# Kernel tuning notes

Hardware: AMD Instinct MI355X
Metric: run time of the kernel (lower is better)

## Reference

```python
import jax, jax.numpy as jnp
import numpy as np
from jax.scipy.linalg import solve_triangular

B, L, HID, NH = 2, 1024, 1024, 4
DK = DV = 256
CONV_K, CHUNK, FIR_S_K, FIR_L_K = 4, 32, 3, 31
GATE_IN = HID + 3 * DV * 4 + DV * 4  # 5120
GATE_H = 2 * DV  # 512


def _l2norm(x):
    return x * jax.lax.rsqrt(jnp.sum(x * x, -1, keepdims=True) + 1e-6)


def _short_conv(x, w):
    # causal depthwise conv1d + silu. x: [b,l,c], w: [c,k]
    c, k = w.shape
    y = jax.lax.conv_general_dilated(x.transpose(0, 2, 1), w[:, None, :], (1,),
                                     [(k - 1, 0)], feature_group_count=c)
    return jax.nn.silu(y.transpose(0, 2, 1))


def _fir(x, f):
    # per-head depthwise causal FIR. x: [b,l,h,d], f: [h,d,k]
    b, l, h, d = x.shape
    k = f.shape[-1]
    xf = x.transpose(0, 2, 3, 1).reshape(b, h * d, l)
    y = jax.lax.conv_general_dilated(xf, f.reshape(h * d, 1, k), (1,),
                                     [(k - 1, 0)], feature_group_count=h * d)
    return y.reshape(b, h, d, l).transpose(0, 3, 1, 2)


def _delta_rule(q, k, v, beta, chunk=CHUNK):
    # q,k: [b,h,L,dk], v: [b,h,L,dv], beta: [b,h,L]; L % chunk == 0
    b, h, l, dk = q.shape
    dv = v.shape[-1]
    n = l // chunk
    q = _l2norm(q)
    k = _l2norm(k)
    v = v * beta[..., None]
    kb = k * beta[..., None]
    rs = lambda t: t.reshape(b, h, n, chunk, -1)
    q, k, v, kb = map(rs, (q, k, v, kb))
    # UT transform: serial forward substitution == unit-lower triangular solve
    A = -jnp.tril(jnp.einsum('bhncd,bhned->bhnce', kb, k), -1)  # strictly lower
    eye = jnp.eye(chunk, dtype=q.dtype)
    T = solve_triangular(eye - A, jnp.broadcast_to(eye, A.shape), lower=True)
    u = T @ v   # [b,h,n,c,dv]
    w = T @ kb  # [b,h,n,c,dk]
    mov = lambda t: jnp.moveaxis(t, 2, 0)

    def step(S, inp):
        qi, ki, ui, wi = inp  # [b,h,c,d]
        attn = jnp.tril(qi @ ki.transpose(0, 1, 3, 2))  # causal incl. diag
        u_i = ui - wi @ S
        o_i = qi @ S + attn @ u_i
        return S + ki.transpose(0, 1, 3, 2) @ u_i, o_i

    S0 = jnp.zeros((b, h, dk, dv), dtype=q.dtype)
    S, o = jax.lax.scan(step, S0, (mov(q), mov(k), mov(u), mov(w)))
    o = jnp.moveaxis(o, 0, 2).reshape(b, h, l, dv)
    return o, S


def _gate(hidden, branches, W1, b1, W2, b2, temp, eps_floor):
    def stats(p):
        m = p.mean(-1, keepdims=True)
        r = jnp.sqrt(jnp.clip((p * p).mean(-1, keepdims=True), 1e-8))
        mx = p.max(-1, keepdims=True)
        return jnp.concatenate([jnp.broadcast_to(m, p.shape),
                                jnp.broadcast_to(r, p.shape),
                                jnp.broadcast_to(mx, p.shape)], -1)

    b, l, h, d = branches[0].shape
    hb = jnp.broadcast_to(hidden[:, :, None, :], (b, l, h, hidden.shape[-1]))
    head_in = jnp.concatenate([hb] + [stats(p) for p in branches] + list(branches), -1)
    hmid = jax.nn.gelu(head_in @ W1 + b1, approximate=False)
    logits = hmid @ W2 + b2  # [b,l,h,4]
    t = jnp.clip(temp, 0.2, 10.0)[None, None, :, None]
    w = jax.nn.softmax(logits / t, -1)
    floor = jnp.clip(eps_floor, 1e-7, 0.1)[None, None]
    w = jnp.maximum(w, floor)
    return w / w.sum(-1, keepdims=True)


def setup_inputs() -> dict:
    key = jax.random.key(0)
    ks = jax.random.split(key, 16)
    s = 0.02
    inp = {
        'x': jax.random.normal(ks[0], (B, L, HID), jnp.float32),
        'Wq': jax.random.normal(ks[1], (HID, NH * DK), jnp.float32) * s,
        'Wk': jax.random.normal(ks[2], (HID, NH * DK), jnp.float32) * s,
        'Wv': jax.random.normal(ks[3], (HID, NH * DV), jnp.float32) * s,
        'Wb': jax.random.normal(ks[4], (HID, NH), jnp.float32) * s,
        'qc_w': jax.random.normal(ks[5], (NH * DK, CONV_K), jnp.float32) * 0.5,
        'kc_w': jax.random.normal(ks[6], (NH * DK, CONV_K), jnp.float32) * 0.5,
        'vc_w': jax.random.normal(ks[7], (NH * DV, CONV_K), jnp.float32) * 0.5,
        'gW1': jax.random.normal(ks[10], (GATE_IN, GATE_H), jnp.float32) * s,
        'gb1': jnp.zeros((GATE_H,), jnp.float32),
        'gW2': jax.random.normal(ks[11], (GATE_H, 4), jnp.float32) * s,
        'gb2': jnp.zeros((4,), jnp.float32),
        'temp': jnp.ones((NH,), jnp.float32),
        'eps_floor': jnp.full((NH, 4), 0.01, jnp.float32),
        'onorm_w': jnp.ones((DV,), jnp.float32),
        'Wo': jax.random.normal(ks[12], (NH * DV, HID), jnp.float32) * s,
    }
    # FIR filters: identity tap at last position + small noise (matches init intent)
    fs = jnp.zeros((NH, DV, FIR_S_K)).at[..., -1].set(1.0)
    fl = jnp.zeros((NH, DV, FIR_L_K)).at[..., -1].set(1.0)
    inp['fir_s'] = fs + s * jax.random.normal(ks[8], fs.shape, jnp.float32)
    inp['fir_l'] = fl + s * jax.random.normal(ks[9], fl.shape, jnp.float32)
    return inp


def reference(x, Wq, Wk, Wv, Wb, qc_w, kc_w, vc_w, fir_s, fir_l,
              gW1, gb1, gW2, gb2, temp, eps_floor, onorm_w, Wo):
    b, l, _ = x.shape
    q = _short_conv(x @ Wq, qc_w).reshape(b, l, NH, DK)
    k = _short_conv(x @ Wk, kc_w).reshape(b, l, NH, DK)
    v = _short_conv(x @ Wv, vc_w).reshape(b, l, NH, DV)
    beta = jax.nn.sigmoid(x @ Wb)  # [b,l,h]
    tr = lambda t: t.transpose(0, 2, 1, 3)
    delta_o, _ = _delta_rule(tr(q), tr(k), tr(v), beta.transpose(0, 2, 1))
    delta_o = tr(delta_o)  # [b,l,h,dv]
    branches = [_fir(v, fir_s), _fir(v, fir_l), delta_o, v]
    w = _gate(x, branches, gW1, gb1, gW2, gb2, temp, eps_floor)
    o = sum(w[..., i:i + 1] * branches[i] for i in range(4))
    o = o * jax.lax.rsqrt((o * o).mean(-1, keepdims=True) + 1e-5) * onorm_w
    return o.reshape(b, l, NH * DV) @ Wo
```

## Files before the change

kernel.cpp:

```cpp
#include <hip/hip_runtime.h>
#include <math.h>

#define BB 2
#define LL 1024
#define HIDD 1024
#define NH 4
#define DD 256
#define NCH 32
#define ROWS 2048
#define HROWS 8192

typedef long long i64;
typedef unsigned short u16t;
typedef unsigned int u32t;
typedef __attribute__((ext_vector_type(8))) short short8;
typedef __attribute__((ext_vector_type(4))) float f32x4;
#define MFMA_BF16(a, b, c) __builtin_amdgcn_mfma_f32_16x16x32_bf16(a, b, c, 0, 0, 0)

__device__ __forceinline__ float sigmoidf_(float x) { return 1.0f / (1.0f + expf(-x)); }

__device__ __forceinline__ u16t f2bf(float f) {
  u32t u = __float_as_uint(f);
  u = u + 0x7FFFu + ((u >> 16) & 1u);
  return (u16t)(u >> 16);
}
__device__ __forceinline__ u32t pk2(u16t a, u16t b) { return (u32t)a | ((u32t)b << 16); }

__device__ __forceinline__ void barrier_lds_only() {
  asm volatile("s_waitcnt lgkmcnt(0)" ::: "memory");
  __builtin_amdgcn_s_barrier();
  asm volatile("" ::: "memory");
}

template<int N>
__device__ __forceinline__ void block_reduce_sum(float* v, float* scratch) {
  int lane = threadIdx.x & 63, wid = threadIdx.x >> 6;
#pragma unroll
  for (int i = 0; i < N; i++) {
    float x = v[i];
#pragma unroll
    for (int off = 1; off < 64; off <<= 1) x += __shfl_xor(x, off);
    if (lane == 0) scratch[wid * N + i] = x;
  }
  __syncthreads();
#pragma unroll
  for (int i = 0; i < N; i++)
    v[i] = scratch[i] + scratch[N + i] + scratch[2 * N + i] + scratch[3 * N + i];
  __syncthreads();
}

template<int N>
__device__ __forceinline__ void block_reduce_max(float* v, float* scratch) {
  int lane = threadIdx.x & 63, wid = threadIdx.x >> 6;
#pragma unroll
  for (int i = 0; i < N; i++) {
    float x = v[i];
#pragma unroll
    for (int off = 1; off < 64; off <<= 1) x = fmaxf(x, __shfl_xor(x, off));
    if (lane == 0) scratch[wid * N + i] = x;
  }
  __syncthreads();
#pragma unroll
  for (int i = 0; i < N; i++)
    v[i] = fmaxf(fmaxf(scratch[i], scratch[N + i]),
                 fmaxf(scratch[2 * N + i], scratch[3 * N + i]));
  __syncthreads();
}

__device__ __forceinline__ void transcast_body(
    const float* __restrict__ in, int ldin, u16t* __restrict__ out, int ldout,
    int nbi, int kbi, float (*tile)[33]) {
  int tx = threadIdx.x & 31, ty = threadIdx.x >> 5;
  int nb = nbi * 32, kb = kbi * 32;
#pragma unroll
  for (int r = 0; r < 4; r++)
    tile[ty + r * 8][tx] = in[(i64)(kb + ty + r * 8) * ldin + nb + tx];
  __syncthreads();
#pragma unroll
  for (int r = 0; r < 4; r++)
    out[(i64)(nb + ty + r * 8) * ldout + kb + tx] = f2bf(tile[tx][ty + r * 8]);
}

__global__ __launch_bounds__(256) void prep_kernel(
    const float* __restrict__ Wq, const float* __restrict__ Wk, const float* __restrict__ Wv,
    const float* __restrict__ x,
    u16t* __restrict__ WqkvT, u16t* __restrict__ xbf) {
  __shared__ float tile[32][33];
  int blk = blockIdx.x, t = threadIdx.x;
  if (blk < 3072) {
    int m = blk >> 10, bi = blk & 1023;
    const float* in = m == 0 ? Wq : m == 1 ? Wk : Wv;
    transcast_body(in, 1024, WqkvT + (i64)m * 1024 * 1024, 1024, bi & 31, bi >> 5, tile);
  } else {
    i64 e = ((i64)(blk - 3072) * 256 + t) * 4;
    float4 v = *(const float4*)(x + e);
    uint2 o;
    o.x = pk2(f2bf(v.x), f2bf(v.y));
    o.y = pk2(f2bf(v.z), f2bf(v.w));
    *(uint2*)(xbf + e) = o;
  }
}

__global__ __launch_bounds__(256) void prep2_kernel(
    const float* __restrict__ gW1, const float* __restrict__ Wo,
    u16t* __restrict__ W1hT, u16t* __restrict__ W1bT, u16t* __restrict__ WoT) {
  __shared__ float tile[32][33];
  int blk = blockIdx.x;
  if (blk < 1024) {
    int which = blk >> 9, bi = blk & 511;
    const float* in = gW1 + (which ? (i64)4096 * 512 : 0);
    transcast_body(in, 512, which ? W1bT : W1hT, 1024, bi & 15, bi >> 4, tile);
  } else {
    int bi = blk - 1024;
    transcast_body(Wo, 1024, WoT, 1024, bi & 31, bi >> 5, tile);
  }
}

__device__ __forceinline__ void gemm_bt_body(
    const u16t* __restrict__ A, const u16t* __restrict__ B,
    float* __restrict__ C, int K, int ldc, int n0, int m0,
    u16t* As, u16t* Bs) {
  int t = threadIdx.x;
  int w = t >> 6, lane = t & 63;
  int l15 = lane & 15, quad = lane >> 4;
  int wm = (w & 1) * 64, wn = (w >> 1) * 64;
  f32x4 acc[4][4] = {};
  int srow = t >> 1, shalf = (t & 1) * 16;
  const u16t* Ag = A + (i64)(m0 + srow) * K + shalf;
  const u16t* Bg = B + (i64)(n0 + srow) * K + shalf;
  for (int k0 = 0; k0 < K; k0 += 32) {
    *(uint4*)&As[srow * 40 + shalf] = *(const uint4*)(Ag + k0);
    *(uint4*)&As[srow * 40 + shalf + 8] = *(const uint4*)(Ag + k0 + 8);
    *(uint4*)&Bs[srow * 40 + shalf] = *(const uint4*)(Bg + k0);
    *(uint4*)&Bs[srow * 40 + shalf + 8] = *(const uint4*)(Bg + k0 + 8);
    __syncthreads();
    short8 a[4], b[4];
#pragma unroll
    for (int mt = 0; mt < 4; mt++)
      a[mt] = *(const short8*)&As[(wm + mt * 16 + l15) * 40 + quad * 8];
#pragma unroll
    for (int nt = 0; nt < 4; nt++)
      b[nt] = *(const short8*)&Bs[(wn + nt * 16 + l15) * 40 + quad * 8];
#pragma unroll
    for (int mt = 0; mt < 4; mt++)
#pragma unroll
      for (int nt = 0; nt < 4; nt++)
        acc[mt][nt] = MFMA_BF16(a[mt], b[nt], acc[mt][nt]);
    __syncthreads();
  }
#pragma unroll
  for (int mt = 0; mt < 4; mt++) {
    int r0 = m0 + wm + mt * 16 + quad * 4;
#pragma unroll
    for (int nt = 0; nt < 4; nt++) {
      int cc = n0 + wn + nt * 16 + l15;
#pragma unroll
      for (int rg = 0; rg < 4; rg++)
        C[(i64)(r0 + rg) * ldc + cc] = acc[mt][nt][rg];
    }
  }
}

__global__ __launch_bounds__(256) void gemm_bt_kernel(
    const u16t* __restrict__ A, const u16t* __restrict__ B,
    float* __restrict__ C, int K, int ldc) {
  __shared__ u16t As[128 * 40];
  __shared__ u16t Bs[128 * 40];
  gemm_bt_body(A, B, C, K, ldc, blockIdx.x * 128, blockIdx.y * 128, As, Bs);
}

__global__ __launch_bounds__(256) void conv_silu3_kernel(
    const float* __restrict__ pre, const float* __restrict__ qw,
    const float* __restrict__ kw, const float* __restrict__ vw,
    float* __restrict__ qo, float* __restrict__ ko, float* __restrict__ vo,
    u16t* __restrict__ brcat) {
  int seg = blockIdx.x >> 13;
  int idx = (blockIdx.x & 8191) * 256 + threadIdx.x;
  int c = idx & 1023, row = idx >> 10, l = row & 1023;
  const float* w = seg == 0 ? qw : seg == 1 ? kw : vw;
  float* out = seg == 0 ? qo : seg == 1 ? ko : vo;
  float4 wv = *(const float4*)(w + c * 4);
  const float* base = pre + (i64)row * 3072 + (seg << 10) + c;
  float acc = wv.w * base[0];
  if (l >= 1) acc += wv.z * base[-3072];
  if (l >= 2) acc += wv.y * base[-2 * 3072];
  if (l >= 3) acc += wv.x * base[-3 * 3072];
  float r = acc * sigmoidf_(acc);
  out[(i64)row * 1024 + c] = r;
  if (seg == 2)
    brcat[((i64)row * 4 + (c >> 8)) * 1024 + 768 + (c & 255)] = f2bf(r);
}

__global__ __launch_bounds__(256) void beta_kernel(
    const float* __restrict__ x, const float* __restrict__ Wb, float* __restrict__ beta) {
  int row = blockIdx.x, t = threadIdx.x;
  __shared__ float sc[16];
  float a[4] = {0, 0, 0, 0};
  for (int c = t; c < 1024; c += 256) {
    float xv = x[(i64)row * 1024 + c];
    float4 wv = *(const float4*)(Wb + c * 4);
    a[0] += xv * wv.x; a[1] += xv * wv.y; a[2] += xv * wv.z; a[3] += xv * wv.w;
  }
  block_reduce_sum<4>(a, sc);
  if (t == 0) {
#pragma unroll
    for (int g = 0; g < 4; g++) beta[row * 4 + g] = sigmoidf_(a[g]);
  }
}

__global__ __launch_bounds__(256) void preprocess_kernel(
    const float* __restrict__ q, const float* __restrict__ k, const float* __restrict__ v,
    const float* __restrict__ beta, float* __restrict__ qn, float* __restrict__ kn,
    float* __restrict__ vb, float* __restrict__ kb, u16t* __restrict__ qnbf) {
  int row = blockIdx.x, t = threadIdx.x;
  __shared__ float sc[8];
  i64 base = (i64)row * 256 + t;
  float qv = q[base], kv = k[base], vv = v[base];
  float vals[2] = {qv * qv, kv * kv};
  block_reduce_sum<2>(vals, sc);
  float qi = rsqrtf(vals[0] + 1e-6f), ki = rsqrtf(vals[1] + 1e-6f);
  float bet = beta[row];
  float qnv = qv * qi, knv = kv * ki;
  qn[base] = qnv;
  kn[base] = knv;
  vb[base] = vv * bet;
  kb[base] = knv * bet;
  int b = row >> 12, l = (row >> 2) & 1023, h = row & 3;
  qnbf[((i64)(b * 4 + h) * 1024 + l) * 256 + t] = f2bf(qnv);
}

__global__ __launch_bounds__(256) void phaseA_kernel(
    const float* __restrict__ qn, const float* __restrict__ kn,
    const float* __restrict__ vb, const float* __restrict__ kb,
    float* __restrict__ u_g, u16t* __restrict__ w_bf, u16t* __restrict__ attn_bf,
    u16t* __restrict__ knT) {
  __shared__ float KN[32][260];
  __shared__ float Ms[32][32];
  int blk = blockIdx.x, t = threadIdx.x;
  int i = blk & 31, bh = blk >> 5;
  int rbase = ((bh >> 2) * LL + i * 32) * NH + (bh & 3);
  i64 bhn = blk;
#pragma unroll
  for (int ii = 0; ii < 8; ii++) {
    int fid = t + ii * 256;
    int c = fid >> 6, dq = (fid & 63) << 2;
    *(float4*)&KN[c][dq] = *(const float4*)(kn + (i64)(rbase + c * NH) * 256 + dq);
  }
  __syncthreads();
  int c = t >> 3, e0 = (t & 7) * 4;
  const float* kbp = kb + (i64)(rbase + c * NH) * 256;
  const float* qp = qn + (i64)(rbase + c * NH) * 256;
  float am[4] = {0, 0, 0, 0}, aa[4] = {0, 0, 0, 0};
  for (int d = 0; d < 256; d += 4) {
    float4 kv = *(const float4*)(kbp + d);
    float4 qv = *(const float4*)(qp + d);
#pragma unroll
    for (int z = 0; z < 4; z++) {
      float4 nv = *(const float4*)&KN[e0 + z][d];
      am[z] += kv.x * nv.x + kv.y * nv.y + kv.z * nv.z + kv.w * nv.w;
      aa[z] += qv.x * nv.x + qv.y * nv.y + qv.z * nv.z + qv.w * nv.w;
    }
  }
  {
    uint2 o;
    u16t a0 = (e0 + 0 <= c) ? f2bf(aa[0]) : 0;
    u16t a1 = (e0 + 1 <= c) ? f2bf(aa[1]) : 0;
    u16t a2 = (e0 + 2 <= c) ? f2bf(aa[2]) : 0;
    u16t a3 = (e0 + 3 <= c) ? f2bf(aa[3]) : 0;
    o.x = pk2(a0, a1); o.y = pk2(a2, a3);
    *(uint2*)(attn_bf + bhn * 1024 + c * 32 + e0) = o;
  }
#pragma unroll
  for (int z = 0; z < 4; z++) {
    int e = e0 + z;
    Ms[c][e] = (e < c) ? am[z] : 0.0f;
  }
  __syncthreads();
  float uc[32], wc[32];
#pragma unroll
  for (int cc = 0; cc < 32; cc++) {
    float uval = vb[(i64)(rbase + cc * NH) * 256 + t];
    float wval = kb[(i64)(rbase + cc * NH) * 256 + t];
#pragma unroll
    for (int c2 = 0; c2 < cc; c2++) {
      float m = Ms[cc][c2];
      uval -= m * uc[c2];
      wval -= m * wc[c2];
    }
    uc[cc] = uval; wc[cc] = wval;
    u_g[(bhn * 32 + cc) * 256 + t] = uval;
    w_bf[(bhn * 32 + cc) * 256 + t] = f2bf(-wval);
  }
  int d = t;
  u16t o[32];
#pragma unroll
  for (int cc = 0; cc < 32; cc++) o[cc] = f2bf(KN[cc][d]);
#pragma unroll
  for (int z = 0; z < 4; z++) {
    uint4 vv;
    vv.x = pk2(o[z * 8 + 0], o[z * 8 + 1]);
    vv.y = pk2(o[z * 8 + 2], o[z * 8 + 3]);
    vv.z = pk2(o[z * 8 + 4], o[z * 8 + 5]);
    vv.w = pk2(o[z * 8 + 6], o[z * 8 + 7]);
    *(uint4*)(knT + (bhn * 256 + d) * 32 + z * 8) = vv;
  }
}

#define SROW 264
struct ScanBuf {
  short8 m8[8];
  f32x4 uc4;
  short8 af;
  short8 kf[4];
};

__device__ void delta_scan_body(
    int blk,
    const u16t* __restrict__ wbf, const u16t* __restrict__ knT,
    const float* __restrict__ u_g, const u16t* __restrict__ qnbf,
    const u16t* __restrict__ attnbf,
    float* __restrict__ dlt, u16t* __restrict__ brcat,
    u16t* Sbf, u16t* Ubf) {
  int t = threadIdx.x, w = t >> 6, lane = t & 63;
  int l15 = lane & 15, quad = lane >> 4;
  int bh = blk & 7, jb = blk >> 3, j0 = jb * 16;
  int b_ = bh >> 2, h_ = bh & 3;
  bool isU = (w < 2);
  int wc = isU ? w : (w - 2);
  for (int idx = t; idx < 16 * SROW; idx += 256) Sbf[idx] = 0;
  f32x4 accS[4] = {};
  __syncthreads();
  __builtin_amdgcn_s_setprio(1);

  auto load_chunk = [&](int i, ScanBuf& B) {
    i64 bhn = (i64)bh * 32 + i;
    const u16t* mbase = isU
        ? wbf + (bhn * 32 + wc * 16 + l15) * 256 + quad * 8
        : qnbf + ((i64)bh * 1024 + i * 32 + wc * 16 + l15) * 256 + quad * 8;
#pragma unroll
    for (int kd = 0; kd < 8; kd++) B.m8[kd] = *(const short8*)(mbase + kd * 32);
    if (isU) {
      int cm = wc * 16 + quad * 4;
#pragma unroll
      for (int r = 0; r < 4; r++)
        B.uc4[r] = u_g[(bhn * 32 + cm + r) * 256 + j0 + l15];
    } else {
      B.af = *(const short8*)(attnbf + bhn * 1024 + (wc * 16 + l15) * 32 + quad * 8);
    }
#pragma unroll
    for (int dt = 0; dt < 4; dt++)
      B.kf[dt] = *(const short8*)(knT + (bhn * 256 + w * 64 + dt * 16 + l15) * 32 + quad * 8);
  };

  auto process = [&](int i, ScanBuf& B) {
    f32x4 zero = {};
    f32x4 ca = isU ? B.uc4 : zero;
    f32x4 cb = zero;
#pragma unroll
    for (int kd = 0; kd < 4; kd++) {
      short8 sfa = *(const short8*)&Sbf[l15 * SROW + kd * 32 + quad * 8];
      short8 sfb = *(const short8*)&Sbf[l15 * SROW + (kd + 4) * 32 + quad * 8];
      ca = MFMA_BF16(B.m8[kd], sfa, ca);
      cb = MFMA_BF16(B.m8[kd + 4], sfb, cb);
    }
    f32x4 cacc;
#pragma unroll
    for (int r = 0; r < 4; r++) cacc[r] = ca[r] + cb[r];
    if (isU) {
      int cm = wc * 16 + quad * 4;
      uint2 o;
      o.x = pk2(f2bf(cacc[0]), f2bf(cacc[1]));
      o.y = pk2(f2bf(cacc[2]), f2bf(cacc[3]));
      *(uint2*)&Ubf[l15 * 40 + cm] = o;
    }
    barrier_lds_only();
    short8 bu = *(const short8*)&Ubf[l15 * 40 + quad * 8];
    if (!isU) {
      cacc = MFMA_BF16(B.af, bu, cacc);
#pragma unroll
      for (int rg = 0; rg < 4; rg++) {
        int l = i * 32 + wc * 16 + quad * 4 + rg;
        i64 row = ((i64)b_ * 1024 + l) * 4 + h_;
        dlt[row * 256 + j0 + l15] = cacc[rg];
        brcat[row * 1024 + 512 + j0 + l15] = f2bf(cacc[rg]);
      }
    }
#pragma unroll
    for (int dt = 0; dt < 4; dt++) accS[dt] = MFMA_BF16(B.kf[dt], bu, accS[dt]);
#pragma unroll
    for (int dt = 0; dt < 4; dt++) {
      uint2 o;
      o.x = pk2(f2bf(accS[dt][0]), f2bf(accS[dt][1]));
      o.y = pk2(f2bf(accS[dt][2]), f2bf(accS[dt][3]));
      *(uint2*)&Sbf[l15 * SROW + w * 64 + dt * 16 + quad * 4] = o;
    }
    barrier_lds_only();
  };

  ScanBuf b0, b1;
  load_chunk(0, b0);
#pragma unroll 1
  for (int ii = 0; ii < 16; ii++) {
    int i = ii * 2;
    load_chunk(i + 1, b1);
    process(i, b0);
    if (ii < 15) load_chunk(i + 2, b0);
    process(i + 1, b1);
  }
  __builtin_amdgcn_s_setprio(0);
}

__device__ void fir2_body(
    int blk, const float* __restrict__ v,
    const float* __restrict__ f_s, const float* __restrict__ f_l,
    float* __restrict__ fs, float* __restrict__ fl, u16t* __restrict__ brcat) {
  int t = threadIdx.x;
  int b = blk >> 8, h = (blk >> 6) & 3, lc = blk & 63;
  int l0 = lc * 16;
  float flw[31], fsw[3];
  const float* flp = f_l + ((i64)h * 256 + t) * 31;
#pragma unroll
  for (int j = 0; j < 31; j++) flw[j] = flp[j];
  const float* fsp = f_s + ((i64)h * 256 + t) * 3;
#pragma unroll
  for (int j = 0; j < 3; j++) fsw[j] = fsp[j];
  float win[46];
#pragma unroll
  for (int r = 0; r < 46; r++) {
    int l = l0 - 30 + r;
    win[r] = (l >= 0) ? v[(((i64)b * 1024 + l) * 4 + h) * 256 + t] : 0.0f;
  }
#pragma unroll
  for (int i = 0; i < 16; i++) {
    float al = 0.0f;
#pragma unroll
    for (int j = 0; j < 31; j++) al += flw[j] * win[i + j];
    float as = fsw[0] * win[i + 28] + fsw[1] * win[i + 29] + fsw[2] * win[i + 30];
    i64 row = ((i64)b * 1024 + (l0 + i)) * 4 + h;
    fs[row * 256 + t] = as;
    fl[row * 256 + t] = al;
    brcat[row * 1024 + t] = f2bf(as);
    brcat[row * 1024 + 256 + t] = f2bf(al);
  }
}

__global__ __launch_bounds__(256) void mega_kernel(
    const u16t* __restrict__ wbf, const u16t* __restrict__ knT,
    const float* __restrict__ u_g, const u16t* __restrict__ qnbf,
    const u16t* __restrict__ attnbf, float* __restrict__ dlt, u16t* __restrict__ brcat,
    const float* __restrict__ vbuf, const float* __restrict__ firs,
    const float* __restrict__ firl, float* __restrict__ fs, float* __restrict__ fl,
    const u16t* __restrict__ xbf, const u16t* __restrict__ W1hT, float* __restrict__ hbase,
    const float* __restrict__ gW1, float* __restrict__ wsum) {
  __shared__ __attribute__((aligned(16))) char smem[20480];
  int blk = blockIdx.x;
  if (blk < 128) {
    u16t* Sbf = (u16t*)smem;
    u16t* Ubf = Sbf + 16 * SROW;
    delta_scan_body(blk, wbf, knT, u_g, qnbf, attnbf, dlt, brcat, Sbf, Ubf);
  } else if (blk < 640) {
    fir2_body(blk - 128, vbuf, firs, firl, fs, fl, brcat);
  } else if (blk < 704) {
    int bi = blk - 640;
    u16t* As = (u16t*)smem;
    u16t* Bs = As + 128 * 40;
    gemm_bt_body(xbf, W1hT, hbase, 1024, 512, (bi & 3) * 128, (bi >> 2) * 128, As, Bs);
  } else {
    int bi = blk - 704;
    int s12 = bi >> 1, col = (bi & 1) * 256 + threadIdx.x;
    const float* p = gW1 + (i64)(1024 + s12 * 256) * 512 + col;
    float acc = 0.0f;
    for (int r = 0; r < 256; r++) acc += p[(i64)r * 512];
    wsum[s12 * 512 + col] = acc;
  }
}

__global__ __launch_bounds__(256) void gatemix_kernel(
    const float* __restrict__ hbase, const float* __restrict__ brW,
    const float* __restrict__ wsum,
    const float* __restrict__ gb1, const float* __restrict__ gW2,
    const float* __restrict__ gb2, const float* __restrict__ temp,
    const float* __restrict__ epsf,
    const float* __restrict__ fs, const float* __restrict__ fl,
    const float* __restrict__ dlt, const float* __restrict__ v,
    const float* __restrict__ onw, u16t* __restrict__ out) {
  int row = blockIdx.x, t = threadIdx.x;
  int bl = row >> 2, h = row & 3;
  __shared__ float sc[32];
  __shared__ float gwsh[4];
  i64 base = (i64)row * 256 + t;
  float bfs = fs[base], bfl = fl[base], bdl = dlt[base], bv = v[base];
  float sums[8] = {bfs, bfs * bfs, bfl, bfl * bfl, bdl, bdl * bdl, bv, bv * bv};
  block_reduce_sum<8>(sums, sc);
  float mx4[4] = {bfs, bfl, bdl, bv};
  block_reduce_max<4>(mx4, sc);
  float st[12];
#pragma unroll
  for (int p = 0; p < 4; p++) {
    st[p * 3 + 0] = sums[p * 2] * (1.0f / 256.0f);
    st[p * 3 + 1] = sqrtf(fmaxf(sums[p * 2 + 1] * (1.0f / 256.0f), 1e-8f));
    st[p * 3 + 2] = mx4[p];
  }
  float lg[4] = {0, 0, 0, 0};
#pragma unroll
  for (int jj = 0; jj < 2; jj++) {
    int o = jj * 256 + t;
    float hm = hbase[(i64)bl * 512 + o] + brW[(i64)row * 512 + o] + gb1[o];
#pragma unroll
    for (int s = 0; s < 12; s++) hm += st[s] * wsum[s * 512 + o];
    float ge = 0.5f * hm * (1.0f + erff(hm * 0.70710678118654752f));
    float4 w2 = *(const float4*)(gW2 + o * 4);
    lg[0] += ge * w2.x; lg[1] += ge * w2.y; lg[2] += ge * w2.z; lg[3] += ge * w2.w;
  }
  block_reduce_sum<4>(lg, sc);
  if (t == 0) {
    float tt = fminf(fmaxf(temp[h], 0.2f), 10.0f);
    float l0 = (lg[0] + gb2[0]) / tt;
    float l1 = (lg[1] + gb2[1]) / tt;
    float l2 = (lg[2] + gb2[2]) / tt;
    float l3 = (lg[3] + gb2[3]) / tt;
    float m = fmaxf(fmaxf(l0, l1), fmaxf(l2, l3));
    float e0 = expf(l0 - m), e1 = expf(l1 - m), e2 = expf(l2 - m), e3 = expf(l3 - m);
    float ssum = e0 + e1 + e2 + e3;
    float w0 = e0 / ssum, w1 = e1 / ssum, w2 = e2 / ssum, w3 = e3 / ssum;
    w0 = fmaxf(w0, fminf(fmaxf(epsf[h * 4 + 0], 1e-7f), 0.1f));
    w1 = fmaxf(w1, fminf(fmaxf(epsf[h * 4 + 1], 1e-7f), 0.1f));
    w2 = fmaxf(w2, fminf(fmaxf(epsf[h * 4 + 2], 1e-7f), 0.1f));
    w3 = fmaxf(w3, fminf(fmaxf(epsf[h * 4 + 3], 1e-7f), 0.1f));
    float s2 = w0 + w1 + w2 + w3;
    gwsh[0] = w0 / s2; gwsh[1] = w1 / s2; gwsh[2] = w2 / s2; gwsh[3] = w3 / s2;
  }
  __syncthreads();
  float g0 = gwsh[0], g1 = gwsh[1], g2 = gwsh[2], g3 = gwsh[3];
  float o = g0 * bfs + g1 * bfl + g2 * bdl + g3 * bv;
  float vals[1] = {o * o};
  block_reduce_sum<1>(vals, sc);
  float scale = rsqrtf(vals[0] * (1.0f / 256.0f) + 1e-5f);
  out[(i64)bl * 1024 + h * 256 + t] = f2bf(o * scale * onw[t]);
}

extern "C" void kernel_launch(void* const* d_in, const int* in_sizes, int n_in,
                              void* d_out, int out_size, void* d_ws, size_t ws_size,
                              hipStream_t stream) {
  (void)in_sizes; (void)n_in; (void)out_size; (void)ws_size;
  const float* x    = (const float*)d_in[0];
  const float* Wq   = (const float*)d_in[1];
  const float* Wk   = (const float*)d_in[2];
  const float* Wv   = (const float*)d_in[3];
  const float* Wb   = (const float*)d_in[4];
  const float* qcw  = (const float*)d_in[5];
  const float* kcw  = (const float*)d_in[6];
  const float* vcw  = (const float*)d_in[7];
  const float* gW1  = (const float*)d_in[8];
  const float* gb1  = (const float*)d_in[9];
  const float* gW2  = (const float*)d_in[10];
  const float* gb2  = (const float*)d_in[11];
  const float* temp = (const float*)d_in[12];
  const float* epsf = (const float*)d_in[13];
  const float* onw  = (const float*)d_in[14];
  const float* Wo   = (const float*)d_in[15];
  const float* firs = (const float*)d_in[16];
  const float* firl = (const float*)d_in[17];
  float* out = (float*)d_out;

  float* ws = (float*)d_ws;
  float* qkv_pre  = ws + 0;
  float* branchW  = ws + 0;
  float* hbase    = ws + 4194304;
  u16t*  brcat    = (u16t*)(ws + 6291456);
  float* qbuf     = ws + 10485760; float* qn = qbuf;
  float* kbuf     = ws + 12582912; float* kn = kbuf;
  float* vbuf     = ws + 14680064;
  float* vb       = ws + 16777216;
  u16t*  omix_bf  = (u16t*)(ws + 16777216);
  u16t*  W1hT     = (u16t*)(ws + 17825792);
  u16t*  W1bT     = (u16t*)(ws + 18087936);
  u16t*  WoT      = (u16t*)(ws + 18350080);
  float* kb       = ws + 18874368;
  float* dlt      = ws + 18874368;
  float* u_g      = ws + 20971520;
  u16t*  w_bf     = (u16t*)(ws + 23068672);
  u16t*  qn_bf    = (u16t*)(ws + 24117248);
  u16t*  knT      = (u16t*)(ws + 25165824);
  u16t*  attn_bf  = (u16t*)(ws + 26214400);
  float* fs       = ws + 26345472;
  float* fl       = ws + 28442624;
  u16t*  xbf      = (u16t*)(ws + 30539776);
  u16t*  WqkvT    = (u16t*)(ws + 31588352);
  float* betab    = ws + 33161216;
  float* wsum     = ws + 33267712;

  prep_kernel<<<5120, 256, 0, stream>>>(Wq, Wk, Wv, x, WqkvT, xbf);
  gemm_bt_kernel<<<dim3(24, 16), 256, 0, stream>>>(xbf, WqkvT, qkv_pre, 1024, 3072);
  conv_silu3_kernel<<<24576, 256, 0, stream>>>(qkv_pre, qcw, kcw, vcw, qbuf, kbuf, vbuf, brcat);
  beta_kernel<<<2048, 256, 0, stream>>>(x, Wb, betab);
  preprocess_kernel<<<8192, 256, 0, stream>>>(qbuf, kbuf, vbuf, betab, qn, kn, vb, kb, qn_bf);
  phaseA_kernel<<<256, 256, 0, stream>>>(qn, kn, vb, kb, u_g, w_bf, attn_bf, knT);
  prep2_kernel<<<2048, 256, 0, stream>>>(gW1, Wo, W1hT, W1bT, WoT);
  mega_kernel<<<728, 256, 0, stream>>>(w_bf, knT, u_g, qn_bf, attn_bf, dlt, brcat,
                                       vbuf, firs, firl, fs, fl,
                                       xbf, W1hT, hbase, gW1, wsum);
  gemm_bt_kernel<<<dim3(4, 64), 256, 0, stream>>>(brcat, W1bT, branchW, 1024, 512);
  gatemix_kernel<<<8192, 256, 0, stream>>>(hbase, branchW, wsum, gb1, gW2, gb2,
                                           temp, epsf, fs, fl, dlt, vbuf, onw, omix_bf);
  gemm_bt_kernel<<<dim3(8, 16), 256, 0, stream>>>(omix_bf, WoT, out, 1024, 1024);
}
```

Measured before the change: 361.5 us.

## Reschedule scan, FIR, weight prep and gate GEMMs; use hardware bf16 pack

Splits the former mega kernel apart. FIR and the weight transpose/cast plus the wsum reduction move into one firprep launch. The delta scan runs alone in its own kernel. The hidden-gate GEMM and the branch GEMM are merged into a single 320-block launch. Inside the scan's serial critical path, the bf16 packing of U and S now uses the v_cvt_pk_bf16_f32 instruction instead of software rounding. The scan no longer overlaps with the FIR and hidden GEMM work, which risks losing concurrency, but the launch count stays the same and the scan blocks no longer share the GPU.

```diff
diff --git a/kernel.cpp b/kernel.cpp
--- a/kernel.cpp
+++ b/kernel.cpp
@@ -25,6 +25,12 @@
   return (u16t)(u >> 16);
 }
 __device__ __forceinline__ u32t pk2(u16t a, u16t b) { return (u32t)a | ((u32t)b << 16); }
+
+__device__ __forceinline__ u32t cvt_pk_bf16(float lo, float hi) {
+  u32t r;
+  asm("v_cvt_pk_bf16_f32 %0, %1, %2" : "=v"(r) : "v"(lo), "v"(hi));
+  return r;
+}
 
 __device__ __forceinline__ void barrier_lds_only() {
   asm volatile("s_waitcnt lgkmcnt(0)" ::: "memory");
@@ -98,21 +104,6 @@
     o.x = pk2(f2bf(v.x), f2bf(v.y));
     o.y = pk2(f2bf(v.z), f2bf(v.w));
     *(uint2*)(xbf + e) = o;
-  }
-}
-
-__global__ __launch_bounds__(256) void prep2_kernel(
-    const float* __restrict__ gW1, const float* __restrict__ Wo,
-    u16t* __restrict__ W1hT, u16t* __restrict__ W1bT, u16t* __restrict__ WoT) {
-  __shared__ float tile[32][33];
-  int blk = blockIdx.x;
-  if (blk < 1024) {
-    int which = blk >> 9, bi = blk & 511;
-    const float* in = gW1 + (which ? (i64)4096 * 512 : 0);
-    transcast_body(in, 512, which ? W1bT : W1hT, 1024, bi & 15, bi >> 4, tile);
-  } else {
-    int bi = blk - 1024;
-    transcast_body(Wo, 1024, WoT, 1024, bi & 31, bi >> 5, tile);
   }
 }
 
@@ -369,8 +360,8 @@
     if (isU) {
       int cm = wc * 16 + quad * 4;
       uint2 o;
-      o.x = pk2(f2bf(cacc[0]), f2bf(cacc[1]));
-      o.y = pk2(f2bf(cacc[2]), f2bf(cacc[3]));
+      o.x = cvt_pk_bf16(cacc[0], cacc[1]);
+      o.y = cvt_pk_bf16(cacc[2], cacc[3]);
       *(uint2*)&Ubf[l15 * 40 + cm] = o;
     }
     barrier_lds_only();
@@ -390,8 +381,8 @@
 #pragma unroll
     for (int dt = 0; dt < 4; dt++) {
       uint2 o;
-      o.x = pk2(f2bf(accS[dt][0]), f2bf(accS[dt][1]));
-      o.y = pk2(f2bf(accS[dt][2]), f2bf(accS[dt][3]));
+      o.x = cvt_pk_bf16(accS[dt][0], accS[dt][1]);
+      o.y = cvt_pk_bf16(accS[dt][2], accS[dt][3]);
       *(uint2*)&Sbf[l15 * SROW + w * 64 + dt * 16 + quad * 4] = o;
     }
     barrier_lds_only();
@@ -410,6 +401,16 @@
   __builtin_amdgcn_s_setprio(0);
 }
 
+__global__ __launch_bounds__(256) void scan_kernel(
+    const u16t* __restrict__ wbf, const u16t* __restrict__ knT,
+    const float* __restrict__ u_g, const u16t* __restrict__ qnbf,
+    const u16t* __restrict__ attnbf,
+    float* __restrict__ dlt, u16t* __restrict__ brcat) {
+  __shared__ __attribute__((aligned(16))) u16t Sbf[16 * SROW];
+  __shared__ __attribute__((aligned(16))) u16t Ubf[16 * 40];
+  delta_scan_body(blockIdx.x, wbf, knT, u_g, qnbf, attnbf, dlt, brcat, Sbf, Ubf);
+}
+
 __device__ void fir2_body(
     int blk, const float* __restrict__ v,
     const float* __restrict__ f_s, const float* __restrict__ f_l,
@@ -444,34 +445,50 @@
   }
 }
 
-__global__ __launch_bounds__(256) void mega_kernel(
-    const u16t* __restrict__ wbf, const u16t* __restrict__ knT,
-    const float* __restrict__ u_g, const u16t* __restrict__ qnbf,
-    const u16t* __restrict__ attnbf, float* __restrict__ dlt, u16t* __restrict__ brcat,
+__global__ __launch_bounds__(256) void firprep_kernel(
     const float* __restrict__ vbuf, const float* __restrict__ firs,
     const float* __restrict__ firl, float* __restrict__ fs, float* __restrict__ fl,
-    const u16t* __restrict__ xbf, const u16t* __restrict__ W1hT, float* __restrict__ hbase,
-    const float* __restrict__ gW1, float* __restrict__ wsum) {
-  __shared__ __attribute__((aligned(16))) char smem[20480];
+    u16t* __restrict__ brcat,
+    const float* __restrict__ gW1, const float* __restrict__ Wo,
+    u16t* __restrict__ W1hT, u16t* __restrict__ W1bT, u16t* __restrict__ WoT,
+    float* __restrict__ wsum) {
+  __shared__ float tile[32][33];
   int blk = blockIdx.x;
-  if (blk < 128) {
-    u16t* Sbf = (u16t*)smem;
-    u16t* Ubf = Sbf + 16 * SROW;
-    delta_scan_body(blk, wbf, knT, u_g, qnbf, attnbf, dlt, brcat, Sbf, Ubf);
-  } else if (blk < 640) {
-    fir2_body(blk - 128, vbuf, firs, firl, fs, fl, brcat);
-  } else if (blk < 704) {
-    int bi = blk - 640;
-    u16t* As = (u16t*)smem;
-    u16t* Bs = As + 128 * 40;
-    gemm_bt_body(xbf, W1hT, hbase, 1024, 512, (bi & 3) * 128, (bi >> 2) * 128, As, Bs);
+  if (blk < 512) {
+    fir2_body(blk, vbuf, firs, firl, fs, fl, brcat);
+  } else if (blk < 2560) {
+    int pb = blk - 512;
+    if (pb < 1024) {
+      int which = pb >> 9, bi = pb & 511;
+      const float* in = gW1 + (which ? (i64)4096 * 512 : 0);
+      transcast_body(in, 512, which ? W1bT : W1hT, 1024, bi & 15, bi >> 4, tile);
+    } else {
+      int bi = pb - 1024;
+      transcast_body(Wo, 1024, WoT, 1024, bi & 31, bi >> 5, tile);
+    }
   } else {
-    int bi = blk - 704;
+    int bi = blk - 2560;
     int s12 = bi >> 1, col = (bi & 1) * 256 + threadIdx.x;
     const float* p = gW1 + (i64)(1024 + s12 * 256) * 512 + col;
     float acc = 0.0f;
     for (int r = 0; r < 256; r++) acc += p[(i64)r * 512];
     wsum[s12 * 512 + col] = acc;
+  }
+}
+
+__global__ __launch_bounds__(256) void gemm2_kernel(
+    const u16t* __restrict__ xbf, const u16t* __restrict__ W1hT,
+    float* __restrict__ hbase,
+    const u16t* __restrict__ brcat, const u16t* __restrict__ W1bT,
+    float* __restrict__ branchW) {
+  __shared__ u16t As[128 * 40];
+  __shared__ u16t Bs[128 * 40];
+  int blk = blockIdx.x;
+  if (blk < 64) {
+    gemm_bt_body(xbf, W1hT, hbase, 1024, 512, (blk & 3) * 128, (blk >> 2) * 128, As, Bs);
+  } else {
+    int bi = blk - 64;
+    gemm_bt_body(brcat, W1bT, branchW, 1024, 512, (bi & 3) * 128, (bi >> 2) * 128, As, Bs);
   }
 }
 
@@ -596,11 +613,10 @@
   beta_kernel<<<2048, 256, 0, stream>>>(x, Wb, betab);
   preprocess_kernel<<<8192, 256, 0, stream>>>(qbuf, kbuf, vbuf, betab, qn, kn, vb, kb, qn_bf);
   phaseA_kernel<<<256, 256, 0, stream>>>(qn, kn, vb, kb, u_g, w_bf, attn_bf, knT);
-  prep2_kernel<<<2048, 256, 0, stream>>>(gW1, Wo, W1hT, W1bT, WoT);
-  mega_kernel<<<728, 256, 0, stream>>>(w_bf, knT, u_g, qn_bf, attn_bf, dlt, brcat,
-                                       vbuf, firs, firl, fs, fl,
-                                       xbf, W1hT, hbase, gW1, wsum);
-  gemm_bt_kernel<<<dim3(4, 64), 256, 0, stream>>>(brcat, W1bT, branchW, 1024, 512);
+  firprep_kernel<<<2584, 256, 0, stream>>>(vbuf, firs, firl, fs, fl, brcat,
+                                           gW1, Wo, W1hT, W1bT, WoT, wsum);
+  scan_kernel<<<128, 256, 0, stream>>>(w_bf, knT, u_g, qn_bf, attn_bf, dlt, brcat);
+  gemm2_kernel<<<320, 256, 0, stream>>>(xbf, W1hT, hbase, brcat, W1bT, branchW);
   gatemix_kernel<<<8192, 256, 0, stream>>>(hbase, branchW, wsum, gb1, gW2, gb2,
                                            temp, epsf, fs, fl, dlt, vbuf, onw, omix_bf);
   gemm_bt_kernel<<<dim3(8, 16), 256, 0, stream>>>(omix_bf, WoT, out, 1024, 1024);
```

Result: slower. 386.7 us (+7.0%).
